# Optimization experiments

Measured on AMD Instinct MI355X. Metric: run time of the kernel, lower is better.

Reference implementation:

```python
import jax, jax.numpy as jnp
import numpy as np

H = 1024
F = 132

def _lstm_cell(x, h, c, Wih, Whh, bih, bhh):
    # PyTorch LSTMCell: gates ordered i, f, g, o
    gates = x @ Wih.T + bih + h @ Whh.T + bhh  # [B, 4H]
    i, f, g, o = jnp.split(gates, 4, axis=-1)
    i = jax.nn.sigmoid(i)
    f = jax.nn.sigmoid(f)
    g = jnp.tanh(g)
    o = jax.nn.sigmoid(o)
    c_new = f * c + i * g
    h_new = o * jnp.tanh(c_new)
    return h_new, c_new


def setup_inputs() -> dict:
    key = jax.random.key(0)
    ks = jax.random.split(key, 16)
    s = 0.02
    return {
        "initial_seq": jax.random.normal(ks[0], (32, 64, F), dtype=jnp.float32),
        "generate_frames_number": 128,
        "W_ih1": jax.random.normal(ks[1], (4 * H, F), dtype=jnp.float32) * s,
        "W_hh1": jax.random.normal(ks[2], (4 * H, H), dtype=jnp.float32) * s,
        "b_ih1": jax.random.normal(ks[3], (4 * H,), dtype=jnp.float32) * s,
        "b_hh1": jax.random.normal(ks[4], (4 * H,), dtype=jnp.float32) * s,
        "W_ih2": jax.random.normal(ks[5], (4 * H, H), dtype=jnp.float32) * s,
        "W_hh2": jax.random.normal(ks[6], (4 * H, H), dtype=jnp.float32) * s,
        "b_ih2": jax.random.normal(ks[7], (4 * H,), dtype=jnp.float32) * s,
        "b_hh2": jax.random.normal(ks[8], (4 * H,), dtype=jnp.float32) * s,
        "W_ih3": jax.random.normal(ks[9], (4 * H, H), dtype=jnp.float32) * s,
        "W_hh3": jax.random.normal(ks[10], (4 * H, H), dtype=jnp.float32) * s,
        "b_ih3": jax.random.normal(ks[11], (4 * H,), dtype=jnp.float32) * s,
        "b_hh3": jax.random.normal(ks[12], (4 * H,), dtype=jnp.float32) * s,
        "W_dec": jax.random.normal(ks[13], (F, H), dtype=jnp.float32) * s,
        "b_dec": jax.random.normal(ks[14], (F,), dtype=jnp.float32) * s,
    }


def reference(initial_seq, generate_frames_number,
              W_ih1, W_hh1, b_ih1, b_hh1,
              W_ih2, W_hh2, b_ih2, b_hh2,
              W_ih3, W_hh3, b_ih3, b_hh3,
              W_dec, b_dec):
    B = initial_seq.shape[0]
    dt = initial_seq.dtype
    zeros = jnp.zeros((B, H), dtype=dt)
    state0 = (zeros, zeros, zeros, zeros, zeros, zeros)  # h0,h1,h2,c0,c1,c2

    def step(state, in_frame):
        h0, h1, h2, c0, c1, c2 = state
        h0, c0 = _lstm_cell(in_frame, h0, c0, W_ih1, W_hh1, b_ih1, b_hh1)
        h1, c1 = _lstm_cell(h0, h1, c1, W_ih2, W_hh2, b_ih2, b_hh2)
        h2, c2 = _lstm_cell(h1, h2, c2, W_ih3, W_hh3, b_ih3, b_hh3)
        out_frame = h2 @ W_dec.T + b_dec  # [B, F]
        return (h0, h1, h2, c0, c1, c2), out_frame

    # Priming pass over the conditioning sequence (outputs discarded except last)
    def prime_step(carry, in_frame):
        state, _ = carry
        state, out = step(state, in_frame)
        return (state, out), None

    init_frame = jnp.zeros((B, F), dtype=dt)
    xs = jnp.swapaxes(initial_seq, 0, 1)  # [T, B, F]
    (state, cur_frame), _ = jax.lax.scan(prime_step, (state0, init_frame), xs)

    def gen_step(carry, _):
        state, frame = carry
        state, out = step(state, frame)
        return (state, out), out

    _, outs = jax.lax.scan(gen_step, (state, cur_frame), None,
                           length=generate_frames_number)  # [N, B, F]
    return jnp.swapaxes(outs, 0, 1)  # [B, N, F]
```

## Files before the change

### kernel.cpp

```cpp
#include <hip/hip_runtime.h>
#include <stdint.h>

typedef unsigned short u16;
typedef unsigned long long u64;
typedef __attribute__((ext_vector_type(8))) short short8;
typedef __attribute__((ext_vector_type(4))) float f32x4;

#define SZ_BIGW    (4096ull*1024ull*2ull)
#define OFF_WHH1   (0ull)
#define OFF_WIH2   (OFF_WHH1 + SZ_BIGW)
#define OFF_WHH2   (OFF_WIH2 + SZ_BIGW)
#define OFF_WIH3   (OFF_WHH2 + SZ_BIGW)
#define OFF_WHH3   (OFF_WIH3 + SZ_BIGW)
#define OFF_MCOMB  (OFF_WHH3 + SZ_BIGW)
#define OFF_WIH1   (OFF_MCOMB + SZ_BIGW)
#define SZ_WIH1    (4096ull*160ull*2ull)
#define OFF_WDECF  (OFF_WIH1 + SZ_WIH1)
#define SZ_WDECF   (160ull*1024ull*2ull)
#define OFF_WDECB  (OFF_WDECF + SZ_WDECF)
#define SZ_WDECB   (1024ull*160ull*2ull)
#define OFF_XPRIM  (OFF_WDECB + SZ_WDECB)
#define SZ_XPRIM   (64ull*5120ull*2ull)
#define OFF_H2HIST (OFF_XPRIM + SZ_XPRIM)
#define SZ_HSLOT   (32768ull*2ull)
#define SZ_H2HIST  (129ull*SZ_HSLOT)
#define OFF_H0R    (OFF_H2HIST + SZ_H2HIST)
#define SZ_HR      (192ull*SZ_HSLOT)
#define OFF_H1R    (OFF_H0R + SZ_HR)
#define OFF_H2R    (OFF_H1R + SZ_HR)
#define SZ_H2R     (64ull*SZ_HSLOT)
#define OFF_ZEROH  (OFF_H2R + SZ_H2R)
#define OFF_FLAGS  (OFF_ZEROH + SZ_HSLOT)
#define SZ_FLAGS   (4096ull)
#define OFF_BS1    (OFF_FLAGS + SZ_FLAGS)
#define OFF_BS1G   (OFF_BS1 + 16384ull)
#define OFF_BS2    (OFF_BS1G + 16384ull)
#define OFF_BS3    (OFF_BS2 + 16384ull)
#define BLOB_SIZE  (OFF_BS3 + 16384ull)

__device__ unsigned char g_blob[BLOB_SIZE];

#define ZERO_BYTES (SZ_HSLOT + SZ_FLAGS)

__device__ __forceinline__ u16 f2bf(float f) {
  unsigned u = __float_as_uint(f);
  u += 0x7fffu + ((u >> 16) & 1u);
  return (u16)(u >> 16);
}
__device__ __forceinline__ float sigm(float x) { return 1.f / (1.f + __expf(-x)); }
__device__ __forceinline__ float tanh_(float x) {
  x = fminf(fmaxf(x, -40.f), 40.f);
  float e = __expf(2.f * x);
  return (e - 1.f) / (e + 1.f);
}

__global__ __launch_bounds__(256) void k_zero(uint4* p, int n) {
  int i = blockIdx.x * 256 + threadIdx.x;
  for (; i < n; i += gridDim.x * 256) p[i] = make_uint4(0u, 0u, 0u, 0u);
}

__global__ __launch_bounds__(256) void k_swizzle(const float* __restrict__ src, u16* __restrict__ dst,
                                                 int J, int Jsrc, int Kpad, int Ksrc, int srcld,
                                                 int transposed, int perm) {
  int total = J * Kpad;
  int nkc = Kpad >> 3;
  for (int o = blockIdx.x * 256 + threadIdx.x; o < total; o += gridDim.x * 256) {
    int chunk = o >> 7, within = o & 127;
    int nt = chunk / nkc, kc = chunk - nt * nkc;
    int jr = within >> 3, ke = within & 7;
    int j = perm ? ((jr >> 2) * 1024 + nt * 4 + (jr & 3)) : (nt * 16 + jr);
    int k = kc * 8 + ke;
    float v = 0.f;
    if (j < Jsrc && k < Ksrc)
      v = transposed ? src[(size_t)k * srcld + j] : src[(size_t)j * srcld + k];
    dst[o] = f2bf(v);
  }
}

__global__ __launch_bounds__(256) void k_xprim(const float* __restrict__ iseq, u16* __restrict__ dst) {
  int o = blockIdx.x * 256 + threadIdx.x;
  if (o >= 64 * 5120) return;
  int t = o / 5120, rem = o - t * 5120;
  int kc = rem >> 8, b = (rem >> 3) & 31, ke = rem & 7;
  int k = kc * 8 + ke;
  float v = (k < 132) ? iseq[(size_t)b * (64 * 132) + t * 132 + k] : 0.f;
  dst[o] = f2bf(v);
}

__global__ __launch_bounds__(256) void k_bias(const float* bih1, const float* bhh1,
                                              const float* bih2, const float* bhh2,
                                              const float* bih3, const float* bhh3,
                                              const float* __restrict__ Wih1, const float* __restrict__ bdec,
                                              float* bs1, float* bs1g, float* bs2, float* bs3) {
  int j = blockIdx.x * 256 + threadIdx.x;
  if (j >= 4096) return;
  float s1 = bih1[j] + bhh1[j];
  float bc = 0.f;
  const float* wr = Wih1 + (size_t)j * 132;
  for (int f = 0; f < 132; ++f) bc += wr[f] * bdec[f];
  bs1[j] = s1;
  bs1g[j] = s1 + bc;
  bs2[j] = bih2[j] + bhh2[j];
  bs3[j] = bih3[j] + bhh3[j];
}

__global__ __launch_bounds__(256) void k_mcomb(const u16* __restrict__ A, const u16* __restrict__ Bm,
                                               u16* __restrict__ dst) {
  int blk = blockIdx.x;
  int mt = blk & 255, jg = blk >> 8;
  int w = threadIdx.x >> 6, l = threadIdx.x & 63, q = l >> 4, r = l & 15;
  int nt = jg * 4 + w;
  f32x4 acc = {};
  for (int ks = 0; ks < 5; ++ks) {
    short8 a = *(const short8*)(A + ((size_t)mt * 20 + ks * 4 + q) * 128 + r * 8);
    short8 b = *(const short8*)(Bm + ((size_t)nt * 20 + ks * 4 + q) * 128 + r * 8);
    acc = __builtin_amdgcn_mfma_f32_16x16x32_bf16(a, b, acc, 0, 0, 0);
  }
  int kout = nt * 16 + r;
#pragma unroll
  for (int i = 0; i < 4; ++i) {
    int jrow = q * 4 + i;
    dst[(((size_t)mt * 128 + (kout >> 3)) << 7) + jrow * 8 + (kout & 7)] = f2bf(acc[i]);
  }
}


__device__ __forceinline__ void wait_all(unsigned* F, unsigned tgt) {
  if (threadIdx.x < 256) {
    while (__hip_atomic_load(F + threadIdx.x, __ATOMIC_RELAXED, __HIP_MEMORY_SCOPE_AGENT) < tgt)
      __builtin_amdgcn_s_sleep(1);
  }
  __syncthreads();
}

__device__ __forceinline__ void layer_step(
    const u16* __restrict__ xa, const u16* __restrict__ Wa, int nsA, int nkcA,
    const u16* __restrict__ xb, const u16* __restrict__ Wb,
    unsigned* waitF, unsigned wtgt,
    const float* __restrict__ bsum, float& creg, u16* __restrict__ hout,
    unsigned* arrF, unsigned aval,
    float (*red)[2][256], u64* hstage, int nt)
{
  int tid = threadIdx.x;
  int w = tid >> 6, l = tid & 63, q = l >> 4, r = l & 15;
  f32x4 acc0 = {}, acc1 = {};

  const u16* wb_base = Wb + (size_t)nt * 128 * 128;
  for (int ks = w; ks < 32; ks += 8) {
    const u16* xp = xb + ks * 1024 + q * 256 + r * 8;
    short8 a0 = *(const short8*)(xp);
    short8 a1 = *(const short8*)(xp + 128);
    short8 bf = *(const short8*)(wb_base + ((size_t)(ks * 4) << 7) + l * 8);
    acc0 = __builtin_amdgcn_mfma_f32_16x16x32_bf16(a0, bf, acc0, 0, 0, 0);
    acc1 = __builtin_amdgcn_mfma_f32_16x16x32_bf16(a1, bf, acc1, 0, 0, 0);
  }

  if (waitF) wait_all(waitF, wtgt);

  const u16* wa_base = Wa + (size_t)nt * nkcA * 128;
  for (int ks = w; ks < nsA; ks += 8) {
    const u16* xp = xa + ks * 1024 + q * 256 + r * 8;
    short8 a0 = *(const short8*)(xp);
    short8 a1 = *(const short8*)(xp + 128);
    short8 bf = *(const short8*)(wa_base + ((size_t)(ks * 4) << 7) + l * 8);
    acc0 = __builtin_amdgcn_mfma_f32_16x16x32_bf16(a0, bf, acc0, 0, 0, 0);
    acc1 = __builtin_amdgcn_mfma_f32_16x16x32_bf16(a1, bf, acc1, 0, 0, 0);
  }

#pragma unroll
  for (int i = 0; i < 4; ++i) { red[w][0][l * 4 + i] = acc0[i]; red[w][1][l * 4 + i] = acc1[i]; }
  __syncthreads();

  if (tid < 128) {
    int b = tid >> 2, hl = tid & 3;
    int mt = b >> 4, row = b & 15;
    int j0 = nt * 4 + hl;
    float g4[4];
#pragma unroll
    for (int g = 0; g < 4; ++g) {
      int col = g * 4 + hl;
      int lidx = ((row >> 2) * 16 + col) * 4 + (row & 3);
      float s = bsum[g * 1024 + j0];
#pragma unroll
      for (int ww = 0; ww < 8; ++ww) s += red[ww][mt][lidx];
      g4[g] = s;
    }
    float iv = sigm(g4[0]), fv = sigm(g4[1]), gv = tanh_(g4[2]), ov = sigm(g4[3]);
    float cn = fv * creg + iv * gv;
    creg = cn;
    ((u16*)hstage)[tid] = f2bf(ov * tanh_(cn));
  }
  __syncthreads();

  if (tid < 64) {
    if (tid < 32) {
      u64 v = hstage[tid];
      u64* dp = (u64*)(hout + ((size_t)(nt >> 1) * 256 + tid * 8 + (nt & 1) * 4));
      __hip_atomic_store(dp, v, __ATOMIC_RELAXED, __HIP_MEMORY_SCOPE_AGENT);
    }
    asm volatile("s_waitcnt vmcnt(0)" ::: "memory");
    if (tid == 0)
      __hip_atomic_store(arrF + nt, aval, __ATOMIC_RELAXED, __HIP_MEMORY_SCOPE_AGENT);
  }
}

__global__ __launch_bounds__(512) void k_rnn(unsigned char* blob) {
  __shared__ float red[8][2][256];
  __shared__ u64 hstage[32];
  const u16* XPRIM = (const u16*)(blob + OFF_XPRIM);
  const u16* tWIH1 = (const u16*)(blob + OFF_WIH1);
  const u16* tMCOMB = (const u16*)(blob + OFF_MCOMB);
  const u16* tWHH1 = (const u16*)(blob + OFF_WHH1);
  const u16* tWIH2 = (const u16*)(blob + OFF_WIH2);
  const u16* tWHH2 = (const u16*)(blob + OFF_WHH2);
  const u16* tWIH3 = (const u16*)(blob + OFF_WIH3);
  const u16* tWHH3 = (const u16*)(blob + OFF_WHH3);
  const float* BS1 = (const float*)(blob + OFF_BS1);
  const float* BS1G = (const float*)(blob + OFF_BS1G);
  const float* BS2 = (const float*)(blob + OFF_BS2);
  const float* BS3 = (const float*)(blob + OFF_BS3);
  u16* H0R = (u16*)(blob + OFF_H0R);
  u16* H1R = (u16*)(blob + OFF_H1R);
  u16* H2R = (u16*)(blob + OFF_H2R);
  u16* H2HIST = (u16*)(blob + OFF_H2HIST);
  const u16* ZEROH = (const u16*)(blob + OFF_ZEROH);
  unsigned* FLAGS = (unsigned*)(blob + OFF_FLAGS);
  unsigned *F1 = FLAGS, *F2 = FLAGS + 256, *F3 = FLAGS + 512;

  int nt = blockIdx.x;
  float c0r = 0.f, c1r = 0.f, c2r = 0.f;

  for (int t = 0; t < 192; ++t) {
    bool prime = t < 64;
    const u16* x0a = prime ? XPRIM + t * 5120 : H2HIST + (size_t)(t - 64) * 32768;
    const u16* h0prev = (t == 0) ? ZEROH : H0R + (size_t)(t - 1) * 32768;
    layer_step(x0a, prime ? tWIH1 : tMCOMB, prime ? 5 : 32, prime ? 20 : 128,
               h0prev, tWHH1,
               prime ? nullptr : F3, (unsigned)t,
               prime ? BS1 : BS1G, c0r, H0R + (size_t)t * 32768,
               F1, (unsigned)(t + 1), red, hstage, nt);
    const u16* h1prev = (t == 0) ? ZEROH : H1R + (size_t)(t - 1) * 32768;
    layer_step(H0R + (size_t)t * 32768, tWIH2, 32, 128,
               h1prev, tWHH2,
               F1, (unsigned)(t + 1),
               BS2, c1r, H1R + (size_t)t * 32768,
               F2, (unsigned)(t + 1), red, hstage, nt);
    const u16* h2prev = (t == 0) ? ZEROH
                      : (t <= 63 ? H2R + (size_t)(t - 1) * 32768
                                 : H2HIST + (size_t)(t - 64) * 32768);
    u16* h2out = (t < 63) ? H2R + (size_t)t * 32768
                          : H2HIST + (size_t)(t - 63) * 32768;
    layer_step(H1R + (size_t)t * 32768, tWIH3, 32, 128,
               h2prev, tWHH3,
               F2, (unsigned)(t + 1),
               BS3, c2r, h2out,
               F3, (unsigned)(t + 1), red, hstage, nt);
  }
}

__global__ __launch_bounds__(256) void k_dec(const u16* __restrict__ h2hist, const u16* __restrict__ Wd,
                                             const float* __restrict__ bdec, float* __restrict__ out) {
  int blk = blockIdx.x;
  int s = blk / 10, nt = blk - s * 10;
  const u16* x = h2hist + (size_t)(s + 1) * 32768;
  int w = threadIdx.x >> 6, l = threadIdx.x & 63, q = l >> 4, r = l & 15;
  f32x4 acc[2] = {};
  for (int ks = w; ks < 32; ks += 4) {
    const u16* xp = x + ks * 1024 + q * 256 + r * 8;
    short8 a0 = *(const short8*)(xp);
    short8 a1 = *(const short8*)(xp + 128);
    short8 bf = *(const short8*)(Wd + (((size_t)nt * 128 + ks * 4) << 7) + l * 8);
    acc[0] = __builtin_amdgcn_mfma_f32_16x16x32_bf16(a0, bf, acc[0], 0, 0, 0);
    acc[1] = __builtin_amdgcn_mfma_f32_16x16x32_bf16(a1, bf, acc[1], 0, 0, 0);
  }
  __shared__ float red[4][2][256];
#pragma unroll
  for (int mt = 0; mt < 2; ++mt)
#pragma unroll
    for (int i = 0; i < 4; ++i) red[w][mt][l * 4 + i] = acc[mt][i];
  __syncthreads();
  for (int pp = threadIdx.x; pp < 512; pp += 256) {
    int b = pp >> 4, fs = pp & 15;
    int mt = b >> 4, row = b & 15;
    int lidx = ((row >> 2) * 16 + fs) * 4 + (row & 3);
    int f = nt * 16 + fs;
    if (f < 132) {
      float v = red[0][mt][lidx] + red[1][mt][lidx] + red[2][mt][lidx] + red[3][mt][lidx] + bdec[f];
      out[(size_t)b * (128 * 132) + s * 132 + f] = v;
    }
  }
}

extern "C" void kernel_launch(void* const* d_in, const int* in_sizes, int n_in,
                              void* d_out, int out_size, void* d_ws, size_t ws_size,
                              hipStream_t stream) {
  unsigned char* blob = nullptr;
  hipGetSymbolAddress((void**)&blob, HIP_SYMBOL(g_blob));

  const float* iseq = (const float*)d_in[0];
  const float* Wih1 = (const float*)d_in[2];
  const float* Whh1 = (const float*)d_in[3];
  const float* bih1 = (const float*)d_in[4];
  const float* bhh1 = (const float*)d_in[5];
  const float* Wih2 = (const float*)d_in[6];
  const float* Whh2 = (const float*)d_in[7];
  const float* bih2 = (const float*)d_in[8];
  const float* bhh2 = (const float*)d_in[9];
  const float* Wih3 = (const float*)d_in[10];
  const float* Whh3 = (const float*)d_in[11];
  const float* bih3 = (const float*)d_in[12];
  const float* bhh3 = (const float*)d_in[13];
  const float* Wdec = (const float*)d_in[14];
  const float* bdec = (const float*)d_in[15];

  u16* tWHH1 = (u16*)(blob + OFF_WHH1);
  u16* tWIH2 = (u16*)(blob + OFF_WIH2);
  u16* tWHH2 = (u16*)(blob + OFF_WHH2);
  u16* tWIH3 = (u16*)(blob + OFF_WIH3);
  u16* tWHH3 = (u16*)(blob + OFF_WHH3);
  u16* tMCOMB = (u16*)(blob + OFF_MCOMB);
  u16* tWIH1 = (u16*)(blob + OFF_WIH1);
  u16* tWDECF = (u16*)(blob + OFF_WDECF);
  u16* tWDECB = (u16*)(blob + OFF_WDECB);
  u16* XPRIM = (u16*)(blob + OFF_XPRIM);
  u16* H2HIST = (u16*)(blob + OFF_H2HIST);
  float* BS1 = (float*)(blob + OFF_BS1);
  float* BS1G = (float*)(blob + OFF_BS1G);
  float* BS2 = (float*)(blob + OFF_BS2);
  float* BS3 = (float*)(blob + OFF_BS3);

  k_zero<<<68, 256, 0, stream>>>((uint4*)(blob + OFF_ZEROH), (int)(ZERO_BYTES / 16));
  k_swizzle<<<2048, 256, 0, stream>>>(Whh1, tWHH1, 4096, 4096, 1024, 1024, 1024, 0, 1);
  k_swizzle<<<2048, 256, 0, stream>>>(Wih2, tWIH2, 4096, 4096, 1024, 1024, 1024, 0, 1);
  k_swizzle<<<2048, 256, 0, stream>>>(Whh2, tWHH2, 4096, 4096, 1024, 1024, 1024, 0, 1);
  k_swizzle<<<2048, 256, 0, stream>>>(Wih3, tWIH3, 4096, 4096, 1024, 1024, 1024, 0, 1);
  k_swizzle<<<2048, 256, 0, stream>>>(Whh3, tWHH3, 4096, 4096, 1024, 1024, 1024, 0, 1);
  k_swizzle<<<2048, 256, 0, stream>>>(Wih1, tWIH1, 4096, 4096, 160, 132, 132, 0, 1);
  k_swizzle<<<512, 256, 0, stream>>>(Wdec, tWDECF, 160, 132, 1024, 1024, 1024, 0, 0);
  k_swizzle<<<512, 256, 0, stream>>>(Wdec, tWDECB, 1024, 1024, 160, 132, 1024, 1, 0);
  k_xprim<<<1280, 256, 0, stream>>>(iseq, XPRIM);
  k_bias<<<16, 256, 0, stream>>>(bih1, bhh1, bih2, bhh2, bih3, bhh3, Wih1, bdec, BS1, BS1G, BS2, BS3);
  k_mcomb<<<4096, 256, 0, stream>>>(tWIH1, tWDECB, tMCOMB);

  {
    void* args[] = { (void*)&blob };
    hipError_t ce = hipLaunchCooperativeKernel((void*)k_rnn, dim3(256), dim3(512), args, 0, stream);
    if (ce != hipSuccess) {
      k_rnn<<<dim3(256), dim3(512), 0, stream>>>(blob);
    }
  }

  k_dec<<<1280, 256, 0, stream>>>(H2HIST, tWDECF, bdec, (float*)d_out);
}
```

Baseline: 2.580 ms.

## Keep recurrent weights resident in LDS and prefetch input weights per layer step

Each persistent block now copies its slices of the three recurrent weight matrices into shared memory once, before the time loop. The input-weight slice for the next layer is loaded into registers while the current layer computes, then written into a rotating LDS buffer after the reduction barrier. This removes repeated global/L2 weight reads from the serial recurrent critical path and overlaps the remaining input-weight fetch with compute. The cost is much higher LDS usage, one block per CU, more register pressure from staging, and an added flag wait in the priming layer-1 step.

New measurement: 2.398 ms. 7.0% less time.

```diff
diff --git a/kernel.cpp b/kernel.cpp
--- a/kernel.cpp
+++ b/kernel.cpp
@@ -133,43 +133,70 @@
   __syncthreads();
 }
 
+template<bool PRIME>
 __device__ __forceinline__ void layer_step(
-    const u16* __restrict__ xa, const u16* __restrict__ Wa, int nsA, int nkcA,
-    const u16* __restrict__ xb, const u16* __restrict__ Wb,
+    const u16* __restrict__ xa,
+    const u16* __restrict__ waG,
+    const u16* __restrict__ segaL,
+    const u16* __restrict__ xb,
+    const u16* __restrict__ wbL,
+    const u16* __restrict__ stage_g,
     unsigned* waitF, unsigned wtgt,
     const float* __restrict__ bsum, float& creg, u16* __restrict__ hout,
     unsigned* arrF, unsigned aval,
-    float (*red)[2][256], u64* hstage, int nt)
+    float (*red)[2][256], u64* hstage, u16* segabuf, int nt)
 {
   int tid = threadIdx.x;
   int w = tid >> 6, l = tid & 63, q = l >> 4, r = l & 15;
   f32x4 acc0 = {}, acc1 = {};
 
-  const u16* wb_base = Wb + (size_t)nt * 128 * 128;
+  short8 st[4];
+  if (stage_g) {
+#pragma unroll
+    for (int i = 0; i < 4; ++i)
+      st[i] = *(const short8*)(stage_g + i * 4096 + tid * 8);
+  }
+
   for (int ks = w; ks < 32; ks += 8) {
     const u16* xp = xb + ks * 1024 + q * 256 + r * 8;
     short8 a0 = *(const short8*)(xp);
     short8 a1 = *(const short8*)(xp + 128);
-    short8 bf = *(const short8*)(wb_base + ((size_t)(ks * 4) << 7) + l * 8);
+    short8 bf = *(const short8*)(wbL + ks * 512 + l * 8);
     acc0 = __builtin_amdgcn_mfma_f32_16x16x32_bf16(a0, bf, acc0, 0, 0, 0);
     acc1 = __builtin_amdgcn_mfma_f32_16x16x32_bf16(a1, bf, acc1, 0, 0, 0);
   }
 
   if (waitF) wait_all(waitF, wtgt);
 
-  const u16* wa_base = Wa + (size_t)nt * nkcA * 128;
-  for (int ks = w; ks < nsA; ks += 8) {
-    const u16* xp = xa + ks * 1024 + q * 256 + r * 8;
-    short8 a0 = *(const short8*)(xp);
-    short8 a1 = *(const short8*)(xp + 128);
-    short8 bf = *(const short8*)(wa_base + ((size_t)(ks * 4) << 7) + l * 8);
-    acc0 = __builtin_amdgcn_mfma_f32_16x16x32_bf16(a0, bf, acc0, 0, 0, 0);
-    acc1 = __builtin_amdgcn_mfma_f32_16x16x32_bf16(a1, bf, acc1, 0, 0, 0);
+  if constexpr (PRIME) {
+    for (int ks = w; ks < 5; ks += 8) {
+      const u16* xp = xa + ks * 1024 + q * 256 + r * 8;
+      short8 a0 = *(const short8*)(xp);
+      short8 a1 = *(const short8*)(xp + 128);
+      short8 bf = *(const short8*)(waG + ((size_t)(ks * 4) << 7) + l * 8);
+      acc0 = __builtin_amdgcn_mfma_f32_16x16x32_bf16(a0, bf, acc0, 0, 0, 0);
+      acc1 = __builtin_amdgcn_mfma_f32_16x16x32_bf16(a1, bf, acc1, 0, 0, 0);
+    }
+  } else {
+    for (int ks = w; ks < 32; ks += 8) {
+      const u16* xp = xa + ks * 1024 + q * 256 + r * 8;
+      short8 a0 = *(const short8*)(xp);
+      short8 a1 = *(const short8*)(xp + 128);
+      short8 bf = *(const short8*)(segaL + ks * 512 + l * 8);
+      acc0 = __builtin_amdgcn_mfma_f32_16x16x32_bf16(a0, bf, acc0, 0, 0, 0);
+      acc1 = __builtin_amdgcn_mfma_f32_16x16x32_bf16(a1, bf, acc1, 0, 0, 0);
+    }
   }
 
 #pragma unroll
   for (int i = 0; i < 4; ++i) { red[w][0][l * 4 + i] = acc0[i]; red[w][1][l * 4 + i] = acc1[i]; }
   __syncthreads();
+
+  if (stage_g) {
+#pragma unroll
+    for (int i = 0; i < 4; ++i)
+      *(short8*)(segabuf + i * 4096 + tid * 8) = st[i];
+  }
 
   if (tid < 128) {
     int b = tid >> 2, hl = tid & 3;
@@ -204,7 +231,9 @@
   }
 }
 
-__global__ __launch_bounds__(512) void k_rnn(unsigned char* blob) {
+__global__ __launch_bounds__(512, 1) void k_rnn(unsigned char* blob) {
+  __shared__ u16 whhL[3][16384];
+  __shared__ u16 segaL[16384];
   __shared__ float red[8][2][256];
   __shared__ u64 hstage[32];
   const u16* XPRIM = (const u16*)(blob + OFF_XPRIM);
@@ -228,33 +257,63 @@
   unsigned *F1 = FLAGS, *F2 = FLAGS + 256, *F3 = FLAGS + 512;
 
   int nt = blockIdx.x;
+  int tid = threadIdx.x;
+  const u16* gWIH1 = tWIH1 + (size_t)nt * 20 * 128;
+  const u16* gMCOMB = tMCOMB + (size_t)nt * 16384;
+  const u16* gWIH2 = tWIH2 + (size_t)nt * 16384;
+  const u16* gWIH3 = tWIH3 + (size_t)nt * 16384;
+
+  {
+    const u16* srcs[4] = { tWHH1 + (size_t)nt * 16384, tWHH2 + (size_t)nt * 16384,
+                           tWHH3 + (size_t)nt * 16384, gWIH2 };
+    u16* dsts[4] = { whhL[0], whhL[1], whhL[2], segaL };
+#pragma unroll
+    for (int tt = 0; tt < 4; ++tt)
+#pragma unroll
+      for (int i = 0; i < 4; ++i)
+        *(short8*)(dsts[tt] + i * 4096 + tid * 8) = *(const short8*)(srcs[tt] + i * 4096 + tid * 8);
+    __syncthreads();
+  }
+
   float c0r = 0.f, c1r = 0.f, c2r = 0.f;
 
-  for (int t = 0; t < 192; ++t) {
-    bool prime = t < 64;
-    const u16* x0a = prime ? XPRIM + t * 5120 : H2HIST + (size_t)(t - 64) * 32768;
+  for (int t = 0; t < 64; ++t) {
     const u16* h0prev = (t == 0) ? ZEROH : H0R + (size_t)(t - 1) * 32768;
-    layer_step(x0a, prime ? tWIH1 : tMCOMB, prime ? 5 : 32, prime ? 20 : 128,
-               h0prev, tWHH1,
-               prime ? nullptr : F3, (unsigned)t,
-               prime ? BS1 : BS1G, c0r, H0R + (size_t)t * 32768,
-               F1, (unsigned)(t + 1), red, hstage, nt);
+    layer_step<true>(XPRIM + t * 5120, gWIH1, nullptr,
+                     h0prev, whhL[0], nullptr,
+                     F3, (unsigned)t,
+                     BS1, c0r, H0R + (size_t)t * 32768,
+                     F1, (unsigned)(t + 1), red, hstage, segaL, nt);
     const u16* h1prev = (t == 0) ? ZEROH : H1R + (size_t)(t - 1) * 32768;
-    layer_step(H0R + (size_t)t * 32768, tWIH2, 32, 128,
-               h1prev, tWHH2,
-               F1, (unsigned)(t + 1),
-               BS2, c1r, H1R + (size_t)t * 32768,
-               F2, (unsigned)(t + 1), red, hstage, nt);
-    const u16* h2prev = (t == 0) ? ZEROH
-                      : (t <= 63 ? H2R + (size_t)(t - 1) * 32768
-                                 : H2HIST + (size_t)(t - 64) * 32768);
-    u16* h2out = (t < 63) ? H2R + (size_t)t * 32768
-                          : H2HIST + (size_t)(t - 63) * 32768;
-    layer_step(H1R + (size_t)t * 32768, tWIH3, 32, 128,
-               h2prev, tWHH3,
-               F2, (unsigned)(t + 1),
-               BS3, c2r, h2out,
-               F3, (unsigned)(t + 1), red, hstage, nt);
+    layer_step<false>(H0R + (size_t)t * 32768, nullptr, segaL,
+                      h1prev, whhL[1], gWIH3,
+                      F1, (unsigned)(t + 1),
+                      BS2, c1r, H1R + (size_t)t * 32768,
+                      F2, (unsigned)(t + 1), red, hstage, segaL, nt);
+    const u16* h2prev = (t == 0) ? ZEROH : H2R + (size_t)(t - 1) * 32768;
+    u16* h2out = (t < 63) ? H2R + (size_t)t * 32768 : H2HIST;
+    layer_step<false>(H1R + (size_t)t * 32768, nullptr, segaL,
+                      h2prev, whhL[2], (t < 63) ? gWIH2 : gMCOMB,
+                      F2, (unsigned)(t + 1),
+                      BS3, c2r, h2out,
+                      F3, (unsigned)(t + 1), red, hstage, segaL, nt);
+  }
+  for (int t = 64; t < 192; ++t) {
+    layer_step<false>(H2HIST + (size_t)(t - 64) * 32768, nullptr, segaL,
+                      H0R + (size_t)(t - 1) * 32768, whhL[0], gWIH2,
+                      F3, (unsigned)t,
+                      BS1G, c0r, H0R + (size_t)t * 32768,
+                      F1, (unsigned)(t + 1), red, hstage, segaL, nt);
+    layer_step<false>(H0R + (size_t)t * 32768, nullptr, segaL,
+                      H1R + (size_t)(t - 1) * 32768, whhL[1], gWIH3,
+                      F1, (unsigned)(t + 1),
+                      BS2, c1r, H1R + (size_t)t * 32768,
+                      F2, (unsigned)(t + 1), red, hstage, segaL, nt);
+    layer_step<false>(H1R + (size_t)t * 32768, nullptr, segaL,
+                      H2HIST + (size_t)(t - 64) * 32768, whhL[2], gMCOMB,
+                      F2, (unsigned)(t + 1),
+                      BS3, c2r, H2HIST + (size_t)(t - 63) * 32768,
+                      F3, (unsigned)(t + 1), red, hstage, segaL, nt);
   }
 }
 
```
